# Kernel tuning notes

Measured on AMD Instinct MI355X. Metric: run time of the kernel, lower is better.

The kernel has to match this reference:

```python
import jax, jax.numpy as jnp
import numpy as np

# ---- static configuration (matches init_kwargs / input_specs) ----
B, T, C = 32, 4096, 3
SCALES = 128
KLF = 10                      # kernel_length_factor
OUT_H, OUT_W = 224, 224
PRECISION = 12
N_PSI = 2 ** PRECISION        # 4096 samples of the integrated wavelet
XMIN, XMAX = -8.0, 8.0        # pywt 'mexh' support
SPAN = XMAX - XMIN
STEP = SPAN / (N_PSI - 1)     # x_master[1] - x_master[0]
MAX_SCALE = T // (2 * KLF)
SCALES_VEC = np.logspace(np.log10(2.0), np.log10(MAX_SCALE), SCALES).astype(np.float32)

# Per-scale gather indices (static: derived from constant scales_vec / x_master grid)
# j = floor(arange(scale*span + 1) / (scale*step)), clipped to valid range.
J_LIST = []
for s in SCALES_VEC:
    s = float(s)
    n = int(np.ceil(s * SPAN + 1.0))
    j = np.floor(np.arange(n, dtype=np.float64) / (s * STEP)).astype(np.int32)
    J_LIST.append(np.clip(j, 0, N_PSI - 1))


def _mexh_int_psi():
    """Integrated Mexican-hat wavelet, exactly as pywt wavefun + CWTLayer build()."""
    x = np.linspace(XMIN, XMAX, N_PSI)
    psi = (2.0 / (np.sqrt(3.0) * np.pi ** 0.25)) * (1.0 - x ** 2) * np.exp(-x ** 2 / 2.0)
    dt = x[1] - x[0]
    int_psi = np.cumsum(psi) * dt
    int_psi -= np.mean(int_psi)
    int_psi /= np.sqrt(np.sum(np.abs(int_psi) ** 2))
    return int_psi.astype(np.float32)


def setup_inputs() -> dict:
    key = jax.random.key(0)
    x = jax.random.normal(key, (B, T, C), dtype=jnp.float32)
    int_psi_base = jnp.asarray(_mexh_int_psi())
    return {"x": x, "int_psi_base": int_psi_base}


def reference(x, int_psi_base):
    pad = min((N_PSI - 1) // 2, T - 1)                       # 2047
    xp = jnp.pad(x, ((0, 0), (pad, pad), (0, 0)), mode="reflect")
    xp = jnp.transpose(xp, (2, 0, 1)).reshape(C * B, T + 2 * pad, 1)  # NWC

    coefs = []
    for s, j in zip(SCALES_VEC, J_LIST):
        # dynamic-length wavelet kernel built by gather, flipped (as in the layer)
        kern = jnp.flip(jnp.take(int_psi_base, jnp.asarray(j), axis=0))[:, None, None]  # (K,1,1) WIO
        conv = jax.lax.conv_general_dilated(
            xp, kern, window_strides=(1,), padding="VALID",
            dimension_numbers=("NWC", "WIO", "NWC"))[..., 0]  # (CB, Lc)
        coef = -jnp.sqrt(jnp.float32(s)) * (conv[:, 1:] - conv[:, :-1])
        d = max((coef.shape[-1] - T) // 2, 0)
        coefs.append(jax.lax.dynamic_slice_in_dim(coef, d, T, axis=1))

    out = jnp.stack(coefs, axis=1)                    # (C*B, SCALES, T)
    out = out.reshape(C, B, SCALES, T).transpose(1, 2, 3, 0)  # (B, SCALES, T, C)
    out = jax.image.resize(out, (B, OUT_H, OUT_W, C), method="bilinear")
    return out
```

## Files before the change

### kernel.cpp

```cpp
#include <hip/hip_runtime.h>
#include <cmath>
#include <cstdint>


constexpr int C_TP     = 8190;
constexpr int C_XROWS  = 8192;
constexpr long long C_HSTRIDE = 3776;
constexpr int C_HGUARD = 160;
constexpr int C_NCLS   = 9;
constexpr int C_RW     = 4;
constexpr int C_NCH    = 56;
constexpr int C_NW     = 224;
constexpr int C_SIGP   = 128;
constexpr int C_M      = 512;
constexpr int C_NP     = 7;
constexpr int C_SL4    = 128;

typedef float v2f __attribute__((ext_vector_type(2)));
typedef float v4f __attribute__((ext_vector_type(4)));

__device__ __forceinline__ void scale_params(int i, float& s32, int& K, int& d, double& a) {
  const double l2   = log10(2.0);
  const double l204 = log10(204.0);
  double step = (l204 - l2) / 127.0;
  double e = (i == 127) ? l204 : ((double)i * step + l2);
  double sv = pow(10.0, e);
  s32 = (float)sv;
  double sp = (double)s32;
  K = (int)ceil(sp * 16.0 + 1.0);
  d = (4094 - K) >> 1;
  a = sp * (16.0 / 4095.0);
}

__global__ void k_build_xp(const float* __restrict__ x, float* __restrict__ xpP) {
  int idx  = blockIdx.x * blockDim.x + threadIdx.x;
  int e    = idx & 3;
  int lane = (idx >> 2) & 63;
  int mp   = idx >> 8;
  int p    = mp * 2 + (e >> 1);
  int s    = lane + 64 * (e & 1);
  float val = 0.f;
  if (s < 96 && p < C_TP) {
    int c = s >> 5;
    int b = s & 31;
    int t = p - 2047;
    if (t < 0) t = -t;
    else if (t > 4095) t = 8190 - t;
    val = x[(b * 4096 + t) * 3 + c];
  }
  xpP[idx] = val;
}

__global__ __launch_bounds__(256) void k_build_H(const float* __restrict__ int_psi,
                                                 float* __restrict__ Hbuf,
                                                 int* __restrict__ meta) {
  int i   = blockIdx.x;
  int cls = blockIdx.y;

  float s32; int K, d; double a;
  scale_params(i, s32, K, d, a);

  int wr = (cls < 7) ? ((cls == 0) ? 7 : cls) : ((cls == 7) ? 0 : 223);
  double ks = 4096.0 / 224.0;
  double sf = ((double)wr + 0.5) * ks - 0.5;
  int t_lo = (int)floor(sf - ks) + 1;
  int t_hi = (int)ceil(sf + ks) - 1;
  if (t_lo < 0) t_lo = 0;
  if (t_hi > 4095) t_hi = 4095;
  int nt  = t_hi - t_lo + 1;
  int npv = nt + 1;

  __shared__ double Wt_sh[40];
  __shared__ double v_sh[64];
  __shared__ float  kern_sh[3352];

  float* rowFull = Hbuf + (long long)(i * C_NCLS + cls) * C_HSTRIDE;
  for (int q = threadIdx.x; q < (int)C_HSTRIDE; q += 256) rowFull[q] = 0.f;

  if (threadIdx.x == 0) {
    double Z = 0.0;
    for (int t = 0; t < nt; ++t) {
      double wv = 1.0 - fabs(sf - (double)(t + t_lo)) / ks;
      if (wv < 0.0) wv = 0.0;
      Wt_sh[t] = wv; Z += wv;
    }
    for (int t = 0; t < nt; ++t) Wt_sh[t] = Wt_sh[t] / Z;
    double sq = sqrt((double)s32);
    for (int q = 0; q <= nt; ++q) {
      double wm1 = (q >= 1)  ? Wt_sh[q - 1] : 0.0;
      double w0  = (q < nt)  ? Wt_sh[q]     : 0.0;
      v_sh[q] = -sq * (wm1 - w0);
    }
  }

  float* kernp = kern_sh + 40;
  int fillN = K + 80;
  for (int q = threadIdx.x; q < fillN; q += 256) {
    int tau = q - 40;
    float kv = 0.f;
    if (tau >= 0 && tau < K) {
      int u = K - 1 - tau;
      int jj = (int)floor((double)u / a);
      jj = jj < 0 ? 0 : (jj > 4095 ? 4095 : jj);
      kv = int_psi[jj];
    }
    kern_sh[q] = kv;
  }
  __syncthreads();

  int p_lo = t_lo + d;
  int Lh   = K + npv - 1;
  int kr   = (cls == 0) ? 1 : ((cls == 8) ? 31 : 0);
  int off0 = p_lo - 128 * kr;
  int shift = off0 & 3;
  int offA  = off0 - shift;
  int rowLen = (shift + Lh + 3) & ~3;

  float* row = Hbuf + (long long)(i * C_NCLS + cls) * C_HSTRIDE + C_HGUARD;
  for (int q = threadIdx.x; q < Lh; q += 256) {
    double acc = 0.0;
    for (int t = 0; t < npv; ++t) acc += v_sh[t] * (double)kernp[q - t];
    row[shift + q] = (float)acc;
  }
  if (threadIdx.x == 0) {
    meta[(i * C_NCLS + cls) * 2 + 0] = offA;
    meta[(i * C_NCLS + cls) * 2 + 1] = rowLen;
  }
}

__global__ __launch_bounds__(64, 8) void k_cwt_main(const float* __restrict__ xpP,
                                                    const float* __restrict__ Hbuf,
                                                    const int* __restrict__ meta,
                                                    float* __restrict__ OT) {
  int piece = blockIdx.x;
  int chunk = blockIdx.y;
  int i     = 127 - blockIdx.z;
  int lane  = threadIdx.x;

  __shared__ v4f Hs[C_RW][C_SL4];

  v2f acc2[C_RW];
  const float* rowP[C_RW];
  int U0 = 0x7fffffff, U1 = 0;
  int startj[C_RW];
#pragma unroll
  for (int j = 0; j < C_RW; ++j) {
    acc2[j] = (v2f){0.f, 0.f};
    int w = chunk * C_RW + j;
    int cls = (w == 0) ? 7 : ((w == 223) ? 8 : (w % 7));
    int k = w / 7;
    int base = i * C_NCLS + cls;
    int offA = meta[base * 2 + 0];
    int rl   = meta[base * 2 + 1];
    int start = offA + 128 * k;
    startj[j] = start;
    if (start < U0) U0 = start;
    if (start + rl > U1) U1 = start + rl;
    rowP[j] = Hbuf + (long long)base * C_HSTRIDE;
  }

  int m0 = U0 + piece * C_M;
  int m1 = m0 + C_M; if (m1 > U1) m1 = U1;
  if (m0 >= m1) return;

  int nIter = (m1 - m0) >> 2;
#pragma unroll
  for (int j = 0; j < C_RW; ++j) {
    const float* src = rowP[j] + (C_HGUARD + m0 - startj[j]);
    for (int q = lane; q < nIter; q += 64)
      Hs[j][q] = *(const v4f*)(src + 4 * q);
  }
  __syncthreads();

  const float* xr = xpP + ((long long)(m0 >> 1) * 256 + lane * 4);
#pragma unroll 2
  for (int it = 0; it < nIter; ++it) {
    v4f xa = *(const v4f*)(xr);
    v4f xb = *(const v4f*)(xr + 256);
    xr += 512;
#pragma unroll
    for (int j = 0; j < C_RW; ++j) {
      v4f h = Hs[j][it];
      acc2[j] += xa.xy * h.x;
      acc2[j] += xa.zw * h.y;
      acc2[j] += xb.xy * h.z;
      acc2[j] += xb.zw * h.w;
    }
  }

#pragma unroll
  for (int j = 0; j < C_RW; ++j) {
    int w = chunk * C_RW + j;
    atomicAdd(&OT[((long long)i * C_NW + w) * C_SIGP + lane],      acc2[j].x);
    atomicAdd(&OT[((long long)i * C_NW + w) * C_SIGP + lane + 64], acc2[j].y);
  }
}

__global__ __launch_bounds__(256) void k_final(const float* __restrict__ OT,
                                               float* __restrict__ out) {
  int wt = blockIdx.x;
  int h  = blockIdx.y;

  float inv = 128.0f / 224.0f;
  float sg = ((float)h + 0.5f) * inv - 0.5f;
  float sgf = floorf(sg);
  int s0 = (int)sgf;
  float fr = sg - sgf;
  int r0, r1;
  if (s0 < 0)        { r0 = 0;   r1 = 0;   fr = 0.f; }
  else if (s0 >= 127){ r0 = 127; r1 = 127; fr = 0.f; }
  else               { r0 = s0;  r1 = s0 + 1; }

  __shared__ float sh0[8 * 132];
  __shared__ float sh1[8 * 132];
  for (int q = threadIdx.x; q < 1024; q += 256) {
    int wp  = q >> 7;
    int sg2 = q & 127;
    int wg  = wt * 8 + wp;
    sh0[wp * 132 + sg2] = OT[((long long)r0 * C_NW + wg) * C_SIGP + sg2];
    sh1[wp * 132 + sg2] = OT[((long long)r1 * C_NW + wg) * C_SIGP + sg2];
  }
  __syncthreads();

  int b  = threadIdx.x >> 3;
  int wp = threadIdx.x & 7;
  int obase = ((b * 224 + h) * 224 + wt * 8 + wp) * 3;
#pragma unroll
  for (int c = 0; c < 3; ++c) {
    int sidx = wp * 132 + c * 32 + b;
    float a0 = sh0[sidx];
    float a1 = sh1[sidx];
    out[obase + c] = (1.0f - fr) * a0 + fr * a1;
  }
}

extern "C" void kernel_launch(void* const* d_in, const int* in_sizes, int n_in,
                              void* d_out, int out_size, void* d_ws, size_t ws_size,
                              hipStream_t stream) {
  const float* x       = (const float*)d_in[0];
  const float* int_psi = (const float*)d_in[1];
  float* out = (float*)d_out;

  float* xpP  = (float*)d_ws;
  float* Hbuf = xpP + (long long)C_XROWS * C_SIGP;
  int*   meta = (int*)(Hbuf + (long long)128 * C_NCLS * C_HSTRIDE);
  float* OT   = (float*)(meta + 2304);

  hipMemsetAsync(OT, 0, (size_t)128 * C_NW * C_SIGP * sizeof(float), stream);
  k_build_xp<<<dim3((C_XROWS / 2 * 256) / 256), dim3(256), 0, stream>>>(x, xpP);
  k_build_H<<<dim3(128, C_NCLS), dim3(256), 0, stream>>>(int_psi, Hbuf, meta);
  k_cwt_main<<<dim3(C_NP, C_NCH, 128), dim3(64), 0, stream>>>(xpP, Hbuf, meta, OT);
  k_final<<<dim3(28, 224), dim3(256), 0, stream>>>(OT, out);
}
```

Baseline: 230.9 us.

## Fuse xp build and OT zeroing into H kernel; widen CWT rows with split-K halves

The reflect-padded input build and the output-accumulator memset move into an extra blockIdx.y slice of the H-building kernel, which removes two launches. The padded signal layout changes to a plain row-major (position, 128 slots) form. The main kernel now processes 8 wavelet rows per block with smaller 256-wide pieces, and splits the piece between two half-waves that are combined by a cross-lane shuffle before the atomics. Each x load is meant to be reused across more output rows, at the cost of lower launch-bounds occupancy and more accumulator registers.

New measurement: 314.3 us. 36.1% more time.

```diff
diff --git a/kernel.cpp b/kernel.cpp
--- a/kernel.cpp
+++ b/kernel.cpp
@@ -8,13 +8,13 @@
 constexpr long long C_HSTRIDE = 3776;
 constexpr int C_HGUARD = 160;
 constexpr int C_NCLS   = 9;
-constexpr int C_RW     = 4;
-constexpr int C_NCH    = 56;
+constexpr int C_RW     = 8;
+constexpr int C_NCH    = 28;
 constexpr int C_NW     = 224;
 constexpr int C_SIGP   = 128;
-constexpr int C_M      = 512;
-constexpr int C_NP     = 7;
-constexpr int C_SL4    = 128;
+constexpr int C_M      = 256;
+constexpr int C_NP     = 14;
+constexpr int C_SQ     = 64;
 
 typedef float v2f __attribute__((ext_vector_type(2)));
 typedef float v4f __attribute__((ext_vector_type(4)));
@@ -32,30 +32,36 @@
   a = sp * (16.0 / 4095.0);
 }
 
-__global__ void k_build_xp(const float* __restrict__ x, float* __restrict__ xpP) {
-  int idx  = blockIdx.x * blockDim.x + threadIdx.x;
-  int e    = idx & 3;
-  int lane = (idx >> 2) & 63;
-  int mp   = idx >> 8;
-  int p    = mp * 2 + (e >> 1);
-  int s    = lane + 64 * (e & 1);
-  float val = 0.f;
-  if (s < 96 && p < C_TP) {
-    int c = s >> 5;
-    int b = s & 31;
-    int t = p - 2047;
-    if (t < 0) t = -t;
-    else if (t > 4095) t = 8190 - t;
-    val = x[(b * 4096 + t) * 3 + c];
-  }
-  xpP[idx] = val;
-}
-
 __global__ __launch_bounds__(256) void k_build_H(const float* __restrict__ int_psi,
+                                                 const float* __restrict__ x,
                                                  float* __restrict__ Hbuf,
-                                                 int* __restrict__ meta) {
+                                                 int* __restrict__ meta,
+                                                 float* __restrict__ xpT,
+                                                 float* __restrict__ OT) {
   int i   = blockIdx.x;
   int cls = blockIdx.y;
+
+  if (cls == 9) {
+    float4* otz = (float4*)OT + (long long)i * 7168;
+    float4 z4 = make_float4(0.f, 0.f, 0.f, 0.f);
+    for (int q = threadIdx.x; q < 7168; q += 256) otz[q] = z4;
+    for (int q = threadIdx.x; q < 8192; q += 256) {
+      int idx  = i * 8192 + q;
+      int slot = idx & 127;
+      int p    = idx >> 7;
+      float val = 0.f;
+      if (slot < 96 && p < C_TP) {
+        int c = slot >> 5;
+        int b = slot & 31;
+        int t = p - 2047;
+        if (t < 0) t = -t;
+        else if (t > 4095) t = 8190 - t;
+        val = x[(b * 4096 + t) * 3 + c];
+      }
+      xpT[idx] = val;
+    }
+    return;
+  }
 
   float s32; int K, d; double a;
   scale_params(i, s32, K, d, a);
@@ -128,7 +134,7 @@
   }
 }
 
-__global__ __launch_bounds__(64, 8) void k_cwt_main(const float* __restrict__ xpP,
+__global__ __launch_bounds__(64, 4) void k_cwt_main(const float* __restrict__ xpT,
                                                     const float* __restrict__ Hbuf,
                                                     const int* __restrict__ meta,
                                                     float* __restrict__ OT) {
@@ -136,16 +142,19 @@
   int chunk = blockIdx.y;
   int i     = 127 - blockIdx.z;
   int lane  = threadIdx.x;
-
-  __shared__ v4f Hs[C_RW][C_SL4];
-
-  v2f acc2[C_RW];
+  int g     = lane & 31;
+  int half  = lane >> 5;
+
+  __shared__ v4f Hs[C_RW][C_SQ];
+
+  v2f accL[C_RW], accH[C_RW];
   const float* rowP[C_RW];
+  int startj[C_RW];
   int U0 = 0x7fffffff, U1 = 0;
-  int startj[C_RW];
 #pragma unroll
   for (int j = 0; j < C_RW; ++j) {
-    acc2[j] = (v2f){0.f, 0.f};
+    accL[j] = (v2f){0.f, 0.f};
+    accH[j] = (v2f){0.f, 0.f};
     int w = chunk * C_RW + j;
     int cls = (w == 0) ? 7 : ((w == 223) ? 8 : (w % 7));
     int k = w / 7;
@@ -163,36 +172,51 @@
   int m1 = m0 + C_M; if (m1 > U1) m1 = U1;
   if (m0 >= m1) return;
 
-  int nIter = (m1 - m0) >> 2;
+  int len = m1 - m0;
+  int nIt = (len + 7) >> 3;
+  int sQ  = 2 * nIt;
+
 #pragma unroll
   for (int j = 0; j < C_RW; ++j) {
     const float* src = rowP[j] + (C_HGUARD + m0 - startj[j]);
-    for (int q = lane; q < nIter; q += 64)
+    for (int q = lane; q < sQ; q += 64)
       Hs[j][q] = *(const v4f*)(src + 4 * q);
   }
   __syncthreads();
 
-  const float* xr = xpP + ((long long)(m0 >> 1) * 256 + lane * 4);
-#pragma unroll 2
-  for (int it = 0; it < nIter; ++it) {
-    v4f xa = *(const v4f*)(xr);
-    v4f xb = *(const v4f*)(xr + 256);
+  const float* xr = xpT + ((long long)(m0 + 4 * nIt * half) << 7) + (g << 2);
+  int hq = half * nIt;
+  for (int it = 0; it < nIt; ++it) {
+    v4f xv0 = *(const v4f*)(xr);
+    v4f xv1 = *(const v4f*)(xr + 128);
+    v4f xv2 = *(const v4f*)(xr + 256);
+    v4f xv3 = *(const v4f*)(xr + 384);
     xr += 512;
 #pragma unroll
     for (int j = 0; j < C_RW; ++j) {
-      v4f h = Hs[j][it];
-      acc2[j] += xa.xy * h.x;
-      acc2[j] += xa.zw * h.y;
-      acc2[j] += xb.xy * h.z;
-      acc2[j] += xb.zw * h.w;
+      v4f h = Hs[j][hq + it];
+      accL[j] += xv0.xy * h.x; accH[j] += xv0.zw * h.x;
+      accL[j] += xv1.xy * h.y; accH[j] += xv1.zw * h.y;
+      accL[j] += xv2.xy * h.z; accH[j] += xv2.zw * h.z;
+      accL[j] += xv3.xy * h.w; accH[j] += xv3.zw * h.w;
     }
   }
 
 #pragma unroll
   for (int j = 0; j < C_RW; ++j) {
-    int w = chunk * C_RW + j;
-    atomicAdd(&OT[((long long)i * C_NW + w) * C_SIGP + lane],      acc2[j].x);
-    atomicAdd(&OT[((long long)i * C_NW + w) * C_SIGP + lane + 64], acc2[j].y);
+    float s0 = accL[j].x, s1 = accL[j].y, s2 = accH[j].x, s3 = accH[j].y;
+    s0 += __shfl_xor(s0, 32);
+    s1 += __shfl_xor(s1, 32);
+    s2 += __shfl_xor(s2, 32);
+    s3 += __shfl_xor(s3, 32);
+    if (lane < 32) {
+      int w = chunk * C_RW + j;
+      float* dst = OT + ((long long)i * C_NW + w) * C_SIGP + (g << 2);
+      atomicAdd(dst + 0, s0);
+      atomicAdd(dst + 1, s1);
+      atomicAdd(dst + 2, s2);
+      atomicAdd(dst + 3, s3);
+    }
   }
 }
 
@@ -241,14 +265,12 @@
   const float* int_psi = (const float*)d_in[1];
   float* out = (float*)d_out;
 
-  float* xpP  = (float*)d_ws;
-  float* Hbuf = xpP + (long long)C_XROWS * C_SIGP;
+  float* xpT  = (float*)d_ws;
+  float* Hbuf = xpT + (long long)C_XROWS * C_SIGP;
   int*   meta = (int*)(Hbuf + (long long)128 * C_NCLS * C_HSTRIDE);
   float* OT   = (float*)(meta + 2304);
 
-  hipMemsetAsync(OT, 0, (size_t)128 * C_NW * C_SIGP * sizeof(float), stream);
-  k_build_xp<<<dim3((C_XROWS / 2 * 256) / 256), dim3(256), 0, stream>>>(x, xpP);
-  k_build_H<<<dim3(128, C_NCLS), dim3(256), 0, stream>>>(int_psi, Hbuf, meta);
-  k_cwt_main<<<dim3(C_NP, C_NCH, 128), dim3(64), 0, stream>>>(xpP, Hbuf, meta, OT);
+  k_build_H<<<dim3(128, 10), dim3(256), 0, stream>>>(int_psi, x, Hbuf, meta, xpT, OT);
+  k_cwt_main<<<dim3(C_NP, C_NCH, 128), dim3(64), 0, stream>>>(xpT, Hbuf, meta, OT);
   k_final<<<dim3(28, 224), dim3(256), 0, stream>>>(OT, out);
 }
```
